# Kernel tuning notes

Hardware: AMD Instinct MI355X
Metric: run time of the kernel (lower is better)

The kernel has to match this reference:

```python
import jax, jax.numpy as jnp
import numpy as np

N, WIDTH, MODES, OUT_CH, N_LAYERS = 131072, 256, 512, 256, 4


def setup_inputs() -> dict:
    key = jax.random.key(0)
    ks = jax.random.split(key, 8)
    scale = 1.0 / (WIDTH * WIDTH)  # matches torch: 1/(in_channels*out_channels)
    return {
        "V": jax.random.normal(ks[0], (N, 3), dtype=jnp.float32),
        "fc0_w": jax.random.normal(ks[1], (WIDTH, 3), dtype=jnp.float32) * 0.02,
        "fc0_b": jnp.zeros((WIDTH,), dtype=jnp.float32),
        # real/imag stacked in last dim -> complex weights (4, in, out, modes)
        "sc_w": jax.random.normal(ks[2], (N_LAYERS, WIDTH, WIDTH, MODES, 2), dtype=jnp.float32) * scale,
        "fc1_w": jax.random.normal(ks[3], (128, WIDTH), dtype=jnp.float32) * 0.02,
        "fc1_b": jnp.zeros((128,), dtype=jnp.float32),
        "fc2_w": jax.random.normal(ks[4], (OUT_CH, 128), dtype=jnp.float32) * 0.02,
        "fc2_b": jnp.zeros((OUT_CH,), dtype=jnp.float32),
    }


def _spectral_conv(x, w_ri):
    # x: (b, c, n) real; w_ri: (c, o, modes, 2) real -> complex (c, o, modes)
    b, c, n = x.shape
    modes = w_ri.shape[2]
    n_freq = n // 2 + 1
    w = jax.lax.complex(w_ri[..., 0], w_ri[..., 1])
    x_ft = jnp.fft.rfft(x, axis=-1)                         # (b, c, n_freq)
    out_modes = jnp.einsum('bcm,com->bom', x_ft[:, :, :modes], w)
    out_ft = jnp.pad(out_modes, ((0, 0), (0, 0), (0, n_freq - modes)))
    return jnp.fft.irfft(out_ft, n=n, axis=-1).astype(x.dtype)


def reference(V, fc0_w, fc0_b, sc_w, fc1_w, fc1_b, fc2_w, fc2_b):
    # lift: (N,3) -> (N,width) -> (1,width,N)
    x = V @ fc0_w.T + fc0_b
    x = x.T[None, :, :]
    for i in range(N_LAYERS):
        x = _spectral_conv(x, sc_w[i])
    feat = x.mean(axis=-1)[0]                                # (width,)
    z = jnp.tanh(feat @ fc1_w.T + fc1_b) @ fc2_w.T + fc2_b   # (out_channels,)
    return z
```

## Files before the change

kernel.cpp:

```cpp
#include <hip/hip_runtime.h>
#include <math.h>


constexpr int kN = 131072;
constexpr int kVsumBlocks = 384;
constexpr int kGatherBlocks = 256;
constexpr size_t kLayerStrideF = (size_t)256 * 256 * 512 * 2;

constexpr size_t WS_WT   = 0;
constexpr size_t WS_PART = 262144;
constexpr size_t WS_X    = 263296;

__global__ __launch_bounds__(256) void vsum(const float* __restrict__ V,
                                            float* __restrict__ ws) {
    int t = threadIdx.x, vb = blockIdx.x;
    int q = vb * 256 + t;
    const float4 v = reinterpret_cast<const float4*>(V)[q];
    int r = q % 3;
    float a[3] = {0.f, 0.f, 0.f};
    a[r] = v.x + v.w;
    a[(r + 1) % 3] = v.y;
    a[(r + 2) % 3] = v.z;
    __shared__ float sred[3][256];
    sred[0][t] = a[0]; sred[1][t] = a[1]; sred[2][t] = a[2];
    __syncthreads();
    for (int off = 128; off > 0; off >>= 1) {
        if (t < off) {
            sred[0][t] += sred[0][t + off];
            sred[1][t] += sred[1][t + off];
            sred[2][t] += sred[2][t + off];
        }
        __syncthreads();
    }
    if (t == 0) {
        float* partials = ws + WS_PART;
        partials[vb * 3 + 0] = sred[0][0];
        partials[vb * 3 + 1] = sred[1][0];
        partials[vb * 3 + 2] = sred[2][0];
    }
}

__global__ __launch_bounds__(256) void gather_lift(const float* __restrict__ sc_w,
                                                   const float* __restrict__ fc0_w,
                                                   const float* __restrict__ fc0_b,
                                                   float* __restrict__ ws) {
    int b = blockIdx.x, t = threadIdx.x;
    if (b < kGatherBlocks) {
        int rem = b * 256 + t;
        int c = rem >> 8, o = rem & 255;
        const float* src = sc_w + (size_t)rem * 1024;
        float w0 = src[0];
        float w1 = src[kLayerStrideF];
        float w2 = src[2 * kLayerStrideF];
        float w3 = src[3 * kLayerStrideF];
        size_t dst = (size_t)o * 256 + c;
        ws[dst]          = w0;
        ws[65536 + dst]  = w1;
        ws[131072 + dst] = w2;
        ws[196608 + dst] = w3;
    } else {
        __shared__ float red[256];
        __shared__ float S[3];
        const float* part = ws + WS_PART;
        for (int j = 0; j < 3; ++j) {
            float a = part[t * 3 + j] + ((t < kVsumBlocks - 256) ? part[(t + 256) * 3 + j] : 0.f);
            red[t] = a;
            __syncthreads();
            for (int off = 128; off > 0; off >>= 1) {
                if (t < off) red[t] += red[t + off];
                __syncthreads();
            }
            if (t == 0) S[j] = red[0];
            __syncthreads();
        }
        ws[WS_X + t] = S[0] * fc0_w[t * 3] + S[1] * fc0_w[t * 3 + 1] +
                       S[2] * fc0_w[t * 3 + 2] + (float)kN * fc0_b[t];
    }
}

__global__ __launch_bounds__(256) void matvec_dc(const float* __restrict__ Wt,
                                                 const float* __restrict__ Xin,
                                                 float* __restrict__ Xout) {
    int o = blockIdx.x, t = threadIdx.x;
    __shared__ float red[256];
    red[t] = Wt[o * 256 + t] * Xin[t];
    __syncthreads();
    for (int off = 128; off > 0; off >>= 1) {
        if (t < off) red[t] += red[t + off];
        __syncthreads();
    }
    if (t == 0) Xout[o] = red[0];
}

__global__ __launch_bounds__(256) void head(const float* __restrict__ X4,
                                            const float* __restrict__ fc1_w,
                                            const float* __restrict__ fc1_b,
                                            const float* __restrict__ fc2_w,
                                            const float* __restrict__ fc2_b,
                                            float* __restrict__ out) {
    __shared__ float feat[256];
    __shared__ float hred[256];
    __shared__ float h[128];
    int t = threadIdx.x;
    feat[t] = X4[t] * (1.0f / (float)kN);
    __syncthreads();
    {
        int j = t & 127, s = t >> 7;
        float acc = 0.f;
        #pragma unroll 8
        for (int i = 0; i < 128; ++i) acc += feat[s * 128 + i] * fc1_w[j * 256 + s * 128 + i];
        hred[s * 128 + j] = acc;
        __syncthreads();
        if (t < 128) h[t] = tanhf(hred[t] + hred[128 + t] + fc1_b[t]);
        __syncthreads();
    }
    float acc = fc2_b[t];
    #pragma unroll 8
    for (int i = 0; i < 128; ++i) acc += h[i] * fc2_w[t * 128 + i];
    out[t] = acc;
}

extern "C" void kernel_launch(void* const* d_in, const int* in_sizes, int n_in,
                              void* d_out, int out_size, void* d_ws, size_t ws_size,
                              hipStream_t stream) {
    const float* V     = (const float*)d_in[0];
    const float* fc0_w = (const float*)d_in[1];
    const float* fc0_b = (const float*)d_in[2];
    const float* sc_w  = (const float*)d_in[3];
    const float* fc1_w = (const float*)d_in[4];
    const float* fc1_b = (const float*)d_in[5];
    const float* fc2_w = (const float*)d_in[6];
    const float* fc2_b = (const float*)d_in[7];
    float* out = (float*)d_out;
    float* ws = (float*)d_ws;

    vsum<<<kVsumBlocks, 256, 0, stream>>>(V, ws);
    gather_lift<<<kGatherBlocks + 1, 256, 0, stream>>>(sc_w, fc0_w, fc0_b, ws);

    float* X = ws + WS_X;
    for (int l = 0; l < 4; ++l) {
        matvec_dc<<<256, 256, 0, stream>>>(ws + (size_t)l * 65536, X + l * 256, X + (l + 1) * 256);
    }
    head<<<1, 256, 0, stream>>>(X + 4 * 256, fc1_w, fc1_b, fc2_w, fc2_b, out);
}
```

Baseline: 37.65 us.

## Pipeline per-layer weight gathers with DC matvecs across fused launches

Replaces the single gather of all four layers' DC weights with per-layer gathers spread across launches. Each launch also runs the matvec for the previous layer, so the scattered weight loads overlap with the dependent chain of small matvecs. The matvec is restructured to 4 blocks of 64 outputs each, reading weights in untransposed [c][o] layout with coalesced access. A block that pre-touches the fc1/fc2 weights to warm the cache is added. Launch count stays at seven, and each launch carries a mix of block roles.

```diff
diff --git a/kernel.cpp b/kernel.cpp
--- a/kernel.cpp
+++ b/kernel.cpp
@@ -3,17 +3,23 @@
 
 
 constexpr int kN = 131072;
-constexpr int kVsumBlocks = 384;
-constexpr int kGatherBlocks = 256;
 constexpr size_t kLayerStrideF = (size_t)256 * 256 * 512 * 2;
 
-constexpr size_t WS_WT   = 0;
-constexpr size_t WS_PART = 262144;
-constexpr size_t WS_X    = 263296;
-
-__global__ __launch_bounds__(256) void vsum(const float* __restrict__ V,
-                                            float* __restrict__ ws) {
-    int t = threadIdx.x, vb = blockIdx.x;
+constexpr size_t W_OFF   = 0;
+constexpr size_t P_OFF   = 262144;
+constexpr size_t X_OFF   = 263296;
+constexpr size_t SCR_OFF = 264576;
+
+__device__ __forceinline__ void gather_one(const float* __restrict__ sc_w,
+                                           float* __restrict__ ws,
+                                           int layer, int idx) {
+    ws[W_OFF + (size_t)layer * 65536 + idx] =
+        sc_w[(size_t)layer * kLayerStrideF + (size_t)idx * 1024];
+}
+
+__device__ __forceinline__ void vsum_block(const float* __restrict__ V,
+                                           float* __restrict__ ws,
+                                           int vb, int t) {
     int q = vb * 256 + t;
     const float4 v = reinterpret_cast<const float4*>(V)[q];
     int r = q % 3;
@@ -33,82 +39,133 @@
         __syncthreads();
     }
     if (t == 0) {
-        float* partials = ws + WS_PART;
+        float* partials = ws + P_OFF;
         partials[vb * 3 + 0] = sred[0][0];
         partials[vb * 3 + 1] = sred[1][0];
         partials[vb * 3 + 2] = sred[2][0];
     }
 }
 
-__global__ __launch_bounds__(256) void gather_lift(const float* __restrict__ sc_w,
-                                                   const float* __restrict__ fc0_w,
-                                                   const float* __restrict__ fc0_b,
-                                                   float* __restrict__ ws) {
-    int b = blockIdx.x, t = threadIdx.x;
-    if (b < kGatherBlocks) {
-        int rem = b * 256 + t;
-        int c = rem >> 8, o = rem & 255;
-        const float* src = sc_w + (size_t)rem * 1024;
-        float w0 = src[0];
-        float w1 = src[kLayerStrideF];
-        float w2 = src[2 * kLayerStrideF];
-        float w3 = src[3 * kLayerStrideF];
-        size_t dst = (size_t)o * 256 + c;
-        ws[dst]          = w0;
-        ws[65536 + dst]  = w1;
-        ws[131072 + dst] = w2;
-        ws[196608 + dst] = w3;
-    } else {
-        __shared__ float red[256];
-        __shared__ float S[3];
-        const float* part = ws + WS_PART;
-        for (int j = 0; j < 3; ++j) {
-            float a = part[t * 3 + j] + ((t < kVsumBlocks - 256) ? part[(t + 256) * 3 + j] : 0.f);
-            red[t] = a;
-            __syncthreads();
-            for (int off = 128; off > 0; off >>= 1) {
-                if (t < off) red[t] += red[t + off];
-                __syncthreads();
-            }
-            if (t == 0) S[j] = red[0];
+__device__ __forceinline__ void lift_block(const float* __restrict__ fc0_w,
+                                           const float* __restrict__ fc0_b,
+                                           float* __restrict__ ws, int t) {
+    __shared__ float red[256];
+    __shared__ float S[3];
+    const float* part = ws + P_OFF;
+    for (int j = 0; j < 3; ++j) {
+        float a = part[t * 3 + j] + ((t < 128) ? part[(t + 256) * 3 + j] : 0.f);
+        red[t] = a;
+        __syncthreads();
+        for (int off = 128; off > 0; off >>= 1) {
+            if (t < off) red[t] += red[t + off];
             __syncthreads();
         }
-        ws[WS_X + t] = S[0] * fc0_w[t * 3] + S[1] * fc0_w[t * 3 + 1] +
-                       S[2] * fc0_w[t * 3 + 2] + (float)kN * fc0_b[t];
-    }
-}
-
-__global__ __launch_bounds__(256) void matvec_dc(const float* __restrict__ Wt,
-                                                 const float* __restrict__ Xin,
-                                                 float* __restrict__ Xout) {
-    int o = blockIdx.x, t = threadIdx.x;
-    __shared__ float red[256];
-    red[t] = Wt[o * 256 + t] * Xin[t];
-    __syncthreads();
-    for (int off = 128; off > 0; off >>= 1) {
-        if (t < off) red[t] += red[t + off];
-        __syncthreads();
-    }
-    if (t == 0) Xout[o] = red[0];
-}
-
-__global__ __launch_bounds__(256) void head(const float* __restrict__ X4,
-                                            const float* __restrict__ fc1_w,
-                                            const float* __restrict__ fc1_b,
-                                            const float* __restrict__ fc2_w,
-                                            const float* __restrict__ fc2_b,
-                                            float* __restrict__ out) {
+        if (t == 0) S[j] = red[0];
+        __syncthreads();
+    }
+    ws[X_OFF + t] = S[0] * fc0_w[t * 3] + S[1] * fc0_w[t * 3 + 1] +
+                    S[2] * fc0_w[t * 3 + 2] + (float)kN * fc0_b[t];
+}
+
+__device__ __forceinline__ void matvec_block(float* __restrict__ ws,
+                                             int layer, int m, int t) {
+    const float* W = ws + W_OFF + (size_t)layer * 65536;
+    const float* Xin = ws + X_OFF + layer * 256;
+    float* Xout = ws + X_OFF + (layer + 1) * 256;
+    __shared__ float xl[256];
+    __shared__ float red[4][64];
+    xl[t] = Xin[t];
+    __syncthreads();
+    int o_l = t & 63, q = t >> 6;
+    int o = m * 64 + o_l;
+    float acc = 0.f;
+    #pragma unroll 8
+    for (int i = 0; i < 64; ++i) {
+        int c = q * 64 + i;
+        acc += W[(size_t)c * 256 + o] * xl[c];
+    }
+    red[q][o_l] = acc;
+    __syncthreads();
+    if (t < 64) Xout[m * 64 + t] = red[0][t] + red[1][t] + red[2][t] + red[3][t];
+}
+
+__device__ __forceinline__ void warm_block(const float* __restrict__ fc1_w,
+                                           const float* __restrict__ fc2_w,
+                                           float* __restrict__ ws, int t) {
+    const float4* f1 = (const float4*)fc1_w;
+    const float4* f2 = (const float4*)fc2_w;
+    float acc = 0.f;
+    for (int i = t; i < 8192; i += 256) {
+        float4 a = f1[i], c = f2[i];
+        acc += a.x + a.y + a.z + a.w + c.x + c.y + c.z + c.w;
+    }
+    ws[SCR_OFF + t] = acc;
+}
+
+__global__ __launch_bounds__(256) void k1(const float* __restrict__ sc_w,
+                                          const float* __restrict__ V,
+                                          float* __restrict__ ws) {
+    int b = blockIdx.x, t = threadIdx.x;
+    if (b < 256) gather_one(sc_w, ws, 0, b * 256 + t);
+    else vsum_block(V, ws, b - 256, t);
+}
+
+__global__ __launch_bounds__(256) void k2(const float* __restrict__ sc_w,
+                                          const float* __restrict__ fc0_w,
+                                          const float* __restrict__ fc0_b,
+                                          float* __restrict__ ws) {
+    int b = blockIdx.x, t = threadIdx.x;
+    if (b < 256) gather_one(sc_w, ws, 1, b * 256 + t);
+    else lift_block(fc0_w, fc0_b, ws, t);
+}
+
+__global__ __launch_bounds__(256) void k3(const float* __restrict__ sc_w,
+                                          const float* __restrict__ fc1_w,
+                                          const float* __restrict__ fc2_w,
+                                          float* __restrict__ ws) {
+    int b = blockIdx.x, t = threadIdx.x;
+    if (b < 128) gather_one(sc_w, ws, 2, b * 256 + t);
+    else if (b < 132) matvec_block(ws, 0, b - 128, t);
+    else warm_block(fc1_w, fc2_w, ws, t);
+}
+
+__global__ __launch_bounds__(256) void k4(const float* __restrict__ sc_w,
+                                          float* __restrict__ ws) {
+    int b = blockIdx.x, t = threadIdx.x;
+    if (b < 128) gather_one(sc_w, ws, 2, 32768 + b * 256 + t);
+    else if (b < 256) gather_one(sc_w, ws, 3, (b - 128) * 256 + t);
+    else matvec_block(ws, 1, b - 256, t);
+}
+
+__global__ __launch_bounds__(256) void k5(const float* __restrict__ sc_w,
+                                          float* __restrict__ ws) {
+    int b = blockIdx.x, t = threadIdx.x;
+    if (b < 128) gather_one(sc_w, ws, 3, 32768 + b * 256 + t);
+    else matvec_block(ws, 2, b - 128, t);
+}
+
+__global__ __launch_bounds__(256) void k6(float* __restrict__ ws) {
+    matvec_block(ws, 3, blockIdx.x, threadIdx.x);
+}
+
+__global__ __launch_bounds__(256) void k7(const float* __restrict__ ws,
+                                          const float* __restrict__ fc1_w,
+                                          const float* __restrict__ fc1_b,
+                                          const float* __restrict__ fc2_w,
+                                          const float* __restrict__ fc2_b,
+                                          float* __restrict__ out) {
     __shared__ float feat[256];
     __shared__ float hred[256];
     __shared__ float h[128];
     int t = threadIdx.x;
-    feat[t] = X4[t] * (1.0f / (float)kN);
+    feat[t] = ws[X_OFF + 4 * 256 + t] * (1.0f / (float)kN);
     __syncthreads();
     {
         int j = t & 127, s = t >> 7;
         float acc = 0.f;
         #pragma unroll 8
-        for (int i = 0; i < 128; ++i) acc += feat[s * 128 + i] * fc1_w[j * 256 + s * 128 + i];
+        for (int i = 0; i < 128; ++i)
+            acc += feat[s * 128 + i] * fc1_w[j * 256 + s * 128 + i];
         hred[s * 128 + j] = acc;
         __syncthreads();
         if (t < 128) h[t] = tanhf(hred[t] + hred[128 + t] + fc1_b[t]);
@@ -134,12 +191,11 @@
     float* out = (float*)d_out;
     float* ws = (float*)d_ws;
 
-    vsum<<<kVsumBlocks, 256, 0, stream>>>(V, ws);
-    gather_lift<<<kGatherBlocks + 1, 256, 0, stream>>>(sc_w, fc0_w, fc0_b, ws);
-
-    float* X = ws + WS_X;
-    for (int l = 0; l < 4; ++l) {
-        matvec_dc<<<256, 256, 0, stream>>>(ws + (size_t)l * 65536, X + l * 256, X + (l + 1) * 256);
-    }
-    head<<<1, 256, 0, stream>>>(X + 4 * 256, fc1_w, fc1_b, fc2_w, fc2_b, out);
-}
+    k1<<<640, 256, 0, stream>>>(sc_w, V, ws);
+    k2<<<257, 256, 0, stream>>>(sc_w, fc0_w, fc0_b, ws);
+    k3<<<133, 256, 0, stream>>>(sc_w, fc1_w, fc2_w, ws);
+    k4<<<260, 256, 0, stream>>>(sc_w, ws);
+    k5<<<132, 256, 0, stream>>>(sc_w, ws);
+    k6<<<4, 256, 0, stream>>>(ws);
+    k7<<<1, 256, 0, stream>>>(ws, fc1_w, fc1_b, fc2_w, fc2_b, out);
+}
```

Result: slower. 48.98 us (+30.1%).
